# Kernel tuning notes

Hardware: AMD Instinct MI355X
Metric: run time of the kernel (lower is better)

Reference implementation:

```python
import jax, jax.numpy as jnp
import numpy as np

B, T, C = 4, 4096, 256

def setup_inputs() -> dict:
    key = jax.random.key(0)
    ks = jax.random.split(key, 7)
    s = 1.0 / np.sqrt(C)
    return {
        "x": jax.random.normal(ks[0], (B, T, C), dtype=jnp.float32),
        "Wq": jax.random.uniform(ks[1], (C, C), jnp.float32, -s, s),
        "bq": jax.random.uniform(ks[2], (C,), jnp.float32, -s, s),
        "Wk": jax.random.uniform(ks[3], (C, C), jnp.float32, -s, s),
        "bk": jax.random.uniform(ks[4], (C,), jnp.float32, -s, s),
        "Wv": jax.random.uniform(ks[5], (C, C), jnp.float32, -s, s),
        "bv": jax.random.uniform(ks[6], (C,), jnp.float32, -s, s),
    }

def reference(x, Wq, bq, Wk, bk, Wv, bv):
    # Projections (torch Linear: y = x @ W^T + b; here W stored as [in,out])
    q = x @ Wq + bq  # [B,T,C]
    k = x @ Wk + bk
    v = x @ Wv + bv
    dk = q.shape[-1]
    scores = jnp.einsum('btc,bsc->bts', q, k) / jnp.sqrt(jnp.float32(dk))
    Tn = x.shape[1]
    causal = jnp.tril(jnp.ones((Tn, Tn), dtype=bool))  # [T,T]
    scores = jnp.where(causal[None, :, :], scores, jnp.float32(-1e9))
    attn = jax.nn.softmax(scores, axis=-1)
    return jnp.einsum('bts,bsc->btc', attn, v)
```

## Files before the change

kernel.cpp:

```cpp
#include <hip/hip_runtime.h>
#include <hip/hip_bf16.h>

#define T_SEQ 4096
#define DIM   256
#define NBATCH 4

typedef short s8v __attribute__((ext_vector_type(8)));
typedef float f4v __attribute__((ext_vector_type(4)));
typedef unsigned short u16;

#define MFMA16(a,b,c) __builtin_amdgcn_mfma_f32_16x16x32_bf16(a,b,c,0,0,0)
#define FENCE_LGKM() asm volatile("s_waitcnt lgkmcnt(0)" ::: "memory")

__device__ int g_cnt[4];

static __device__ __forceinline__ u16 f2bf(float f) {
  union { float f; unsigned int u; } c; c.f = f;
  unsigned int u = c.u;
  unsigned int r = (u + 0x7fffu + ((u >> 16) & 1u)) >> 16;
  return (u16)r;
}

static __device__ __forceinline__ s8v pack8(const float* p) {
  float4 a = *(const float4*)p;
  float4 b = *(const float4*)(p + 4);
  s8v r;
  r[0] = (short)f2bf(a.x); r[1] = (short)f2bf(a.y);
  r[2] = (short)f2bf(a.z); r[3] = (short)f2bf(a.w);
  r[4] = (short)f2bf(b.x); r[5] = (short)f2bf(b.y);
  r[6] = (short)f2bf(b.z); r[7] = (short)f2bf(b.w);
  return r;
}

static __device__ __forceinline__ void gll16(const u16* g, u16* l) {
  __builtin_amdgcn_global_load_lds(
      (const __attribute__((address_space(1))) unsigned int*)g,
      (__attribute__((address_space(3))) unsigned int*)l, 16, 0, 0);
}

__global__ void diag_fill_kernel(float* __restrict__ out, float val, int n) {
  int i = blockIdx.x * blockDim.x + threadIdx.x;
  if (i < n) out[i] = val;
}

__global__ void wtrans_kernel(const float* __restrict__ Wq, const float* __restrict__ Wk,
                              const float* __restrict__ Wv, u16* __restrict__ Wt) {
  if (blockIdx.x == 0 && blockIdx.y == 0 && blockIdx.z == 0 &&
      threadIdx.y == 0 && threadIdx.x < 4)
    g_cnt[threadIdx.x] = 0;
  __shared__ float tile[32][33];
  int m = blockIdx.z;
  const float* W = (m == 0) ? Wq : ((m == 1) ? Wk : Wv);
  int bx = blockIdx.x * 32, by = blockIdx.y * 32;
  int x = threadIdx.x, y = threadIdx.y;
  #pragma unroll
  for (int i = 0; i < 32; i += 8) tile[y + i][x] = W[(by + y + i) * DIM + bx + x];
  __syncthreads();
  u16* o = Wt + m * DIM * DIM;
  #pragma unroll
  for (int i = 0; i < 32; i += 8) o[(bx + y + i) * DIM + by + x] = f2bf(tile[x][y + i]);
}

__global__ __launch_bounds__(256) void proj_kernel(
    const float* __restrict__ x, const u16* __restrict__ Wt,
    const float* __restrict__ bq, const float* __restrict__ bk, const float* __restrict__ bv,
    u16* __restrict__ qf, u16* __restrict__ kf, u16* __restrict__ vf) {
  alignas(16) __shared__ u16 Kl[64 * 264];
  alignas(16) __shared__ u16 Vl[256 * 72];

  int bid = blockIdx.x;
  int which = blockIdx.y;
  int tid  = threadIdx.x;
  int wave = tid >> 6, lane = tid & 63, quad = lane >> 4, l16 = lane & 15;
  int row0 = bid * 64 + wave * 16;

  s8v a[8];
  const float* xp = x + (size_t)(row0 + l16) * DIM + quad * 8;
  #pragma unroll
  for (int ks = 0; ks < 8; ks++) a[ks] = pack8(xp + ks * 32);

  if (which == 0) {
    const u16* W = Wt + DIM * DIM;
    f4v acc[16];
    #pragma unroll
    for (int nt = 0; nt < 16; nt++) acc[nt] = (f4v){0.f, 0.f, 0.f, 0.f};
    #pragma unroll
    for (int ks = 0; ks < 8; ks++) {
      #pragma unroll
      for (int nt = 0; nt < 16; nt++) {
        s8v bfr = *(const s8v*)(W + (nt * 16 + l16) * DIM + ks * 32 + quad * 8);
        acc[nt] = MFMA16(a[ks], bfr, acc[nt]);
      }
    }
    #pragma unroll
    for (int nt = 0; nt < 16; nt++) {
      float bb = bk[nt * 16 + l16];
      #pragma unroll
      for (int r = 0; r < 4; r++)
        Kl[(wave * 16 + quad * 4 + r) * 264 + nt * 16 + l16] = f2bf(acc[nt][r] + bb);
    }
    __syncthreads();
    #pragma unroll
    for (int i = 0; i < 8; i++) {
      int o = tid + i * 256;
      int tile = o >> 10, rem = o & 1023;
      int f = rem >> 6, ln = rem & 63;
      int sl = tile * 32 + (f >> 3) * 16 + (ln & 15);
      int c  = (f & 7) * 32 + (ln >> 4) * 8;
      s8v v = *(const s8v*)&Kl[sl * 264 + c];
      *(s8v*)&kf[(((size_t)(bid * 2 + tile) * 16 + f) * 64 + ln) * 8] = v;
    }
  } else if (which == 1) {
    const u16* W = Wt + 2 * DIM * DIM;
    f4v acc[16];
    #pragma unroll
    for (int nt = 0; nt < 16; nt++) acc[nt] = (f4v){0.f, 0.f, 0.f, 0.f};
    #pragma unroll
    for (int ks = 0; ks < 8; ks++) {
      #pragma unroll
      for (int nt = 0; nt < 16; nt++) {
        s8v bfr = *(const s8v*)(W + (nt * 16 + l16) * DIM + ks * 32 + quad * 8);
        acc[nt] = MFMA16(a[ks], bfr, acc[nt]);
      }
    }
    #pragma unroll
    for (int nt = 0; nt < 16; nt++) {
      float bb = bv[nt * 16 + l16];
      union { u16 h[4]; uint2 v2; } pk;
      #pragma unroll
      for (int r = 0; r < 4; r++) pk.h[r] = f2bf(acc[nt][r] + bb);
      *(uint2*)&Vl[(nt * 16 + l16) * 72 + wave * 16 + quad * 4] = pk.v2;
    }
    __syncthreads();
    #pragma unroll
    for (int i = 0; i < 8; i++) {
      int o = tid + i * 256;
      int tile = o >> 10, rem = o & 1023;
      int nt = rem >> 6, ln = rem & 63;
      int c  = nt * 16 + (ln & 15);
      int sl = tile * 32 + (ln >> 4) * 8;
      s8v v = *(const s8v*)&Vl[c * 72 + sl];
      *(s8v*)&vf[(((size_t)(bid * 2 + tile) * 16 + nt) * 64 + ln) * 8] = v;
    }
  } else {
    const u16* W = Wt;
    f4v acc[16];
    #pragma unroll
    for (int nt = 0; nt < 16; nt++) acc[nt] = (f4v){0.f, 0.f, 0.f, 0.f};
    #pragma unroll
    for (int ks = 0; ks < 8; ks++) {
      #pragma unroll
      for (int nt = 0; nt < 16; nt++) {
        s8v bfr = *(const s8v*)(W + (nt * 16 + l16) * DIM + ks * 32 + quad * 8);
        acc[nt] = MFMA16(a[ks], bfr, acc[nt]);
      }
    }
    #pragma unroll
    for (int nt = 0; nt < 16; nt++) {
      float bb = bq[nt * 16 + l16];
      #pragma unroll
      for (int r = 0; r < 4; r++)
        Kl[(wave * 16 + quad * 4 + r) * 264 + nt * 16 + l16] =
            f2bf((acc[nt][r] + bb) * 0.0625f);
    }
    __syncthreads();
    #pragma unroll
    for (int i = 0; i < 8; i++) {
      int o = tid + i * 256;
      int row = o >> 5, c8 = (o & 31) * 8;
      s8v v = *(const s8v*)&Kl[row * 264 + c8];
      int colp = (c8 + ((row & 31) << 3)) & 255;
      *(s8v*)&qf[(size_t)(bid * 64 + row) * 256 + colp] = v;
    }
  }
}

__global__ __launch_bounds__(1024, 4) void attn_kernel(
    const u16* __restrict__ qf, const u16* __restrict__ kf, const u16* __restrict__ vf,
    float* __restrict__ Opart, float* __restrict__ lpart, float* __restrict__ out) {
  alignas(16) __shared__ u16 Qs[32768];
  alignas(16) __shared__ u16 KVa[16384];
  alignas(16) __shared__ u16 KVb[16384];
  alignas(16) __shared__ u16 Ps[16 * 640];
  __shared__ int taskS;

  int bid = blockIdx.x, b = bid & 3;
  int tid = threadIdx.x;
  int w = tid >> 6, lane = tid & 63, quad = lane >> 4, l16 = lane & 15;
  int s = w >> 1, h = w & 1;

  const u16* qfb = qf + (size_t)b * T_SEQ * DIM;
  const u16* kfb = kf + (size_t)b * 128 * 8192;
  const u16* vfb = vf + (size_t)b * 128 * 8192;

  int qrow = (s << 4) + l16;
  int qbase = qrow << 8;
  int qrot = (qrow & 31) << 3;

  for (;;) {
    if (tid == 0) taskS = atomicAdd(&g_cnt[b], 1);
    __syncthreads();
    int t = taskS;
    if (t >= 80) break;
    int q, c;
    if (t < 8)        { q = 24 + t;        c = 0; }
    else if (t < 16)  { q = 24 + (t - 8);  c = 1; }
    else if (t < 24)  { q = 24 + (t - 16); c = 2; }
    else if (t == 24) { q = 31;            c = 3; }
    else if (t < 33)  { q = 16 + (t - 25); c = 0; }
    else if (t < 41)  { q = 16 + (t - 33); c = 1; }
    else if (t == 41) { q = 23;            c = 2; }
    else if (t < 50)  { q = 8 + (t - 42);  c = 0; }
    else if (t == 50) { q = 15;            c = 1; }
    else if (t == 51) { q = 7;             c = 0; }
    else { int u = t - 52, sz = u >> 2, band = u & 3;
           if (band == 0)      { q = 6 - sz;  c = 0; }
           else if (band == 1) { q = 14 - sz; c = 1; }
           else if (band == 2) { q = 22 - sz; c = 2; }
           else                { q = 30 - sz; c = 3; } }
    int row0 = q * 128;
    int n = 4 * q + 4;
    int lo = c * 32, hi = min(n, lo + 32);
    int nch = (q + 8) >> 3;

    {
      const u16* qsrc = qfb + ((size_t)row0 << 8) + (w << 11) + (lane << 3);
      u16* qdst = &Qs[w << 11];
      #pragma unroll
      for (int i = 0; i < 4; i++) gll16(qsrc + (i << 9), qdst + (i << 9));
      const u16* kt = kfb + ((size_t)lo << 13);
      const u16* vt = vfb + ((size_t)lo << 13);
      gll16(kt + (w << 9) + (lane << 3), &KVa[w << 9]);
      gll16(vt + (w << 9) + (lane << 3), &KVa[8192 + (w << 9)]);
    }
    __syncthreads();

    int rowBase = row0 + (s << 4);
    f4v o[8];
    #pragma unroll
    for (int nt = 0; nt < 8; nt++) o[nt] = (f4v){0.f, 0.f, 0.f, 0.f};
    float lrow[4] = {0.f, 0.f, 0.f, 0.f};

    auto iter_body = [&](const u16* buf, int kvi) {
      f4v c0 = (f4v){0.f, 0.f, 0.f, 0.f}, c1 = (f4v){0.f, 0.f, 0.f, 0.f};
      #pragma unroll
      for (int ks = 0; ks < 8; ks++) {
        s8v qa = *(const s8v*)&Qs[qbase + ((ks * 32 + (quad << 3) + qrot) & 255)];
        s8v k0 = *(const s8v*)&buf[(ks << 9) + (lane << 3)];
        s8v k1 = *(const s8v*)&buf[((8 + ks) << 9) + (lane << 3)];
        c0 = MFMA16(qa, k0, c0);
        c1 = MFMA16(qa, k1, c1);
      }
      int s0 = kvi * 32 + l16;
      #pragma unroll
      for (int r = 0; r < 4; r++) {
        int tq = rowBase + (quad << 2) + r;
        float v0 = (s0 > tq)      ? -1e30f : c0[r];
        float v1 = (s0 + 16 > tq) ? -1e30f : c1[r];
        float p0 = __expf(v0);
        float p1 = __expf(v1);
        Ps[w * 640 + ((quad << 2) + r) * 40 + l16]      = f2bf(p0);
        Ps[w * 640 + ((quad << 2) + r) * 40 + 16 + l16] = f2bf(p1);
        lrow[r] += p0 + p1;
      }
      FENCE_LGKM();
      s8v pa = *(const s8v*)&Ps[w * 640 + l16 * 40 + (quad << 3)];
      #pragma unroll
      for (int nt = 0; nt < 8; nt++) {
        s8v vfr = *(const s8v*)&buf[8192 + (((h << 3) + nt) << 9) + (lane << 3)];
        o[nt] = MFMA16(pa, vfr, o[nt]);
      }
    };

    #pragma unroll 1
    for (int kv = lo; kv < hi; kv += 2) {
      {
        const u16* kt = kfb + ((size_t)(kv + 1) << 13);
        const u16* vt = vfb + ((size_t)(kv + 1) << 13);
        gll16(kt + (w << 9) + (lane << 3), &KVb[w << 9]);
        gll16(vt + (w << 9) + (lane << 3), &KVb[8192 + (w << 9)]);
      }
      iter_body(KVa, kv);
      __syncthreads();
      if (kv + 2 < hi) {
        const u16* kt = kfb + ((size_t)(kv + 2) << 13);
        const u16* vt = vfb + ((size_t)(kv + 2) << 13);
        gll16(kt + (w << 9) + (lane << 3), &KVa[w << 9]);
        gll16(vt + (w << 9) + (lane << 3), &KVa[8192 + (w << 9)]);
      }
      iter_body(KVb, kv + 1);
      __syncthreads();
    }

    #pragma unroll
    for (int r = 0; r < 4; r++) {
      #pragma unroll
      for (int d = 1; d < 16; d <<= 1) lrow[r] += __shfl_xor(lrow[r], d);
    }

    if (nch == 1) {
      float inv[4];
      #pragma unroll
      for (int r = 0; r < 4; r++) inv[r] = 1.0f / lrow[r];
      #pragma unroll
      for (int nt = 0; nt < 8; nt++) {
        #pragma unroll
        for (int r = 0; r < 4; r++)
          out[(size_t)(b * T_SEQ + rowBase + (quad << 2) + r) * DIM +
              ((h * 8 + nt) * 16 + l16)] = o[nt][r] * inv[r];
      }
    } else {
      int slotB = (q < 16) ? (q - 8) * 2
                : (q < 24) ? 16 + (q - 16) * 3
                           : 40 + (q - 24) * 4;
      int slot = b * 72 + slotB + c;
      float* Op = Opart + ((size_t)slot << 15);
      #pragma unroll
      for (int nt = 0; nt < 8; nt++) {
        #pragma unroll
        for (int r = 0; r < 4; r++)
          Op[((s << 4) + (quad << 2) + r) * 256 + (h * 8 + nt) * 16 + l16] = o[nt][r];
      }
      if (h == 0 && l16 == 0) {
        #pragma unroll
        for (int r = 0; r < 4; r++)
          lpart[slot * 128 + (s << 4) + (quad << 2) + r] = lrow[r];
      }
    }
  }
}

__global__ void combine_kernel(const float* __restrict__ Opart,
                               const float* __restrict__ lpart,
                               float* __restrict__ out) {
  int blk = blockIdx.x;
  int b = blk & 3;
  int rest = blk >> 2;
  int q = 8 + (rest >> 3);
  int g = rest & 7;
  int col = threadIdx.x;
  int nch = (q + 8) >> 3;
  int slotB = (q < 16) ? (q - 8) * 2
            : (q < 24) ? 16 + (q - 16) * 3
                       : 40 + (q - 24) * 4;
  int slot0 = b * 72 + slotB;
  #pragma unroll 4
  for (int i = 0; i < 16; i++) {
    int rt = g * 16 + i;
    float acc = 0.f, ls = 0.f;
    for (int c = 0; c < nch; c++) {
      acc += Opart[(((size_t)(slot0 + c)) << 15) + rt * 256 + col];
      ls  += lpart[(slot0 + c) * 128 + rt];
    }
    out[(size_t)(b * T_SEQ + q * 128 + rt) * DIM + col] = acc / ls;
  }
}

extern "C" void kernel_launch(void* const* d_in, const int* in_sizes, int n_in,
                              void* d_out, int out_size, void* d_ws, size_t ws_size,
                              hipStream_t stream) {
  const float* x  = (const float*)d_in[0];
  const float* Wq = (const float*)d_in[1];
  const float* bq = (const float*)d_in[2];
  const float* Wk = (const float*)d_in[3];
  const float* bk = (const float*)d_in[4];
  const float* Wv = (const float*)d_in[5];
  const float* bv = (const float*)d_in[6];

  const size_t NTD = (size_t)NBATCH * T_SEQ * DIM;
  const size_t WT_ELEMS = (size_t)3 * DIM * DIM;
  const size_t NSLOT = 288;
  const size_t REQ_BYTES = (WT_ELEMS + 3 * NTD) * sizeof(u16)
                         + NSLOT * 32768 * sizeof(float)
                         + NSLOT * 128 * sizeof(float);

  if (ws_size < REQ_BYTES) {
    float val = (float)(ws_size >> 20);
    diag_fill_kernel<<<(out_size + 255) / 256, 256, 0, stream>>>((float*)d_out, val, out_size);
    return;
  }

  u16* ws = (u16*)d_ws;
  u16* WT = ws;
  u16* Kf = ws + WT_ELEMS;
  u16* Vf = Kf + NTD;
  u16* Qf = Vf + NTD;
  float* Opart = (float*)(Qf + NTD);
  float* lpart = Opart + NSLOT * 32768;

  wtrans_kernel<<<dim3(8, 8, 3), dim3(32, 8, 1), 0, stream>>>(Wq, Wk, Wv, WT);
  proj_kernel<<<dim3(256, 3, 1), dim3(256, 1, 1), 0, stream>>>(x, WT, bq, bk, bv, Qf, Kf, Vf);
  attn_kernel<<<dim3(256, 1, 1), dim3(1024, 1, 1), 0, stream>>>(Qf, Kf, Vf,
                                                                Opart, lpart, (float*)d_out);
  combine_kernel<<<dim3(768, 1, 1), dim3(256, 1, 1), 0, stream>>>(Opart, lpart, (float*)d_out);
}
```

Baseline: 227.9 us.

## Split QK^T across wave pairs and keep Q fragments in registers

The Q projection now writes Q in a pre-swizzled MFMA fragment layout, so each wave loads its eight Q fragments directly into registers and the Q shared-memory tile disappears. The two waves in a pair now each compute half of the 32 score columns instead of both computing all of them. This removes the duplicated QK^T MFMAs and the Q LDS reads, and frees shared memory. In exchange it adds a workgroup-wide s_barrier inside every KV iteration so the shared P tile is complete, and it merges row sums from the two halves through LDS.

```diff
diff --git a/kernel.cpp b/kernel.cpp
--- a/kernel.cpp
+++ b/kernel.cpp
@@ -167,10 +167,12 @@
     #pragma unroll
     for (int i = 0; i < 8; i++) {
       int o = tid + i * 256;
-      int row = o >> 5, c8 = (o & 31) * 8;
-      s8v v = *(const s8v*)&Kl[row * 264 + c8];
-      int colp = (c8 + ((row & 31) << 3)) & 255;
-      *(s8v*)&qf[(size_t)(bid * 64 + row) * 256 + colp] = v;
+      int tile = o >> 10, rem = o & 1023;
+      int f = rem >> 6, ln = rem & 63;
+      int sl = tile * 32 + (f >> 3) * 16 + (ln & 15);
+      int c  = (f & 7) * 32 + (ln >> 4) * 8;
+      s8v v = *(const s8v*)&Kl[sl * 264 + c];
+      *(s8v*)&qf[(((size_t)(bid * 2 + tile) * 16 + f) * 64 + ln) * 8] = v;
     }
   }
 }
@@ -178,10 +180,10 @@
 __global__ __launch_bounds__(1024, 4) void attn_kernel(
     const u16* __restrict__ qf, const u16* __restrict__ kf, const u16* __restrict__ vf,
     float* __restrict__ Opart, float* __restrict__ lpart, float* __restrict__ out) {
-  alignas(16) __shared__ u16 Qs[32768];
   alignas(16) __shared__ u16 KVa[16384];
   alignas(16) __shared__ u16 KVb[16384];
-  alignas(16) __shared__ u16 Ps[16 * 640];
+  alignas(16) __shared__ u16 Ps[8 * 640];
+  __shared__ float lbuf[8][2][16];
   __shared__ int taskS;
 
   int bid = blockIdx.x, b = bid & 3;
@@ -189,13 +191,9 @@
   int w = tid >> 6, lane = tid & 63, quad = lane >> 4, l16 = lane & 15;
   int s = w >> 1, h = w & 1;
 
-  const u16* qfb = qf + (size_t)b * T_SEQ * DIM;
+  const u16* qfb = qf + (size_t)b * 128 * 8192;
   const u16* kfb = kf + (size_t)b * 128 * 8192;
   const u16* vfb = vf + (size_t)b * 128 * 8192;
-
-  int qrow = (s << 4) + l16;
-  int qbase = qrow << 8;
-  int qrot = (qrow & 31) << 3;
 
   for (;;) {
     if (tid == 0) taskS = atomicAdd(&g_cnt[b], 1);
@@ -223,11 +221,14 @@
     int lo = c * 32, hi = min(n, lo + 32);
     int nch = (q + 8) >> 3;
 
+    s8v qa[8];
     {
-      const u16* qsrc = qfb + ((size_t)row0 << 8) + (w << 11) + (lane << 3);
-      u16* qdst = &Qs[w << 11];
-      #pragma unroll
-      for (int i = 0; i < 4; i++) gll16(qsrc + (i << 9), qdst + (i << 9));
+      const u16* qt = qfb + (((size_t)(q * 4 + (s >> 1)) * 16 + (s & 1) * 8) * 64) * 8;
+      #pragma unroll
+      for (int ks = 0; ks < 8; ks++) qa[ks] = *(const s8v*)(qt + (ks * 64 + lane) * 8);
+    }
+
+    {
       const u16* kt = kfb + ((size_t)lo << 13);
       const u16* vt = vfb + ((size_t)lo << 13);
       gll16(kt + (w << 9) + (lane << 3), &KVa[w << 9]);
@@ -242,29 +243,25 @@
     float lrow[4] = {0.f, 0.f, 0.f, 0.f};
 
     auto iter_body = [&](const u16* buf, int kvi) {
-      f4v c0 = (f4v){0.f, 0.f, 0.f, 0.f}, c1 = (f4v){0.f, 0.f, 0.f, 0.f};
+      f4v cc = (f4v){0.f, 0.f, 0.f, 0.f};
       #pragma unroll
       for (int ks = 0; ks < 8; ks++) {
-        s8v qa = *(const s8v*)&Qs[qbase + ((ks * 32 + (quad << 3) + qrot) & 255)];
-        s8v k0 = *(const s8v*)&buf[(ks << 9) + (lane << 3)];
-        s8v k1 = *(const s8v*)&buf[((8 + ks) << 9) + (lane << 3)];
-        c0 = MFMA16(qa, k0, c0);
-        c1 = MFMA16(qa, k1, c1);
-      }
-      int s0 = kvi * 32 + l16;
+        s8v kfr = *(const s8v*)&buf[(((h << 3) + ks) << 9) + (lane << 3)];
+        cc = MFMA16(qa[ks], kfr, cc);
+      }
+      int s0 = kvi * 32 + (h << 4) + l16;
       #pragma unroll
       for (int r = 0; r < 4; r++) {
         int tq = rowBase + (quad << 2) + r;
-        float v0 = (s0 > tq)      ? -1e30f : c0[r];
-        float v1 = (s0 + 16 > tq) ? -1e30f : c1[r];
-        float p0 = __expf(v0);
-        float p1 = __expf(v1);
-        Ps[w * 640 + ((quad << 2) + r) * 40 + l16]      = f2bf(p0);
-        Ps[w * 640 + ((quad << 2) + r) * 40 + 16 + l16] = f2bf(p1);
-        lrow[r] += p0 + p1;
+        float p = __expf((s0 > tq) ? -1e30f : cc[r]);
+        Ps[s * 640 + ((quad << 2) + r) * 40 + (h << 4) + l16] = f2bf(p);
+        lrow[r] += p;
       }
       FENCE_LGKM();
-      s8v pa = *(const s8v*)&Ps[w * 640 + l16 * 40 + (quad << 3)];
+      __builtin_amdgcn_sched_barrier(0);
+      __builtin_amdgcn_s_barrier();
+      __builtin_amdgcn_sched_barrier(0);
+      s8v pa = *(const s8v*)&Ps[s * 640 + l16 * 40 + (quad << 3)];
       #pragma unroll
       for (int nt = 0; nt < 8; nt++) {
         s8v vfr = *(const s8v*)&buf[8192 + (((h << 3) + nt) << 9) + (lane << 3)];
@@ -297,17 +294,21 @@
       #pragma unroll
       for (int d = 1; d < 16; d <<= 1) lrow[r] += __shfl_xor(lrow[r], d);
     }
+    if (l16 == 0) {
+      #pragma unroll
+      for (int r = 0; r < 4; r++) lbuf[s][h][(quad << 2) + r] = lrow[r];
+    }
+    __syncthreads();
 
     if (nch == 1) {
-      float inv[4];
-      #pragma unroll
-      for (int r = 0; r < 4; r++) inv[r] = 1.0f / lrow[r];
       #pragma unroll
       for (int nt = 0; nt < 8; nt++) {
         #pragma unroll
-        for (int r = 0; r < 4; r++)
+        for (int r = 0; r < 4; r++) {
+          float ls = lbuf[s][0][(quad << 2) + r] + lbuf[s][1][(quad << 2) + r];
           out[(size_t)(b * T_SEQ + rowBase + (quad << 2) + r) * DIM +
-              ((h * 8 + nt) * 16 + l16)] = o[nt][r] * inv[r];
+              ((h * 8 + nt) * 16 + l16)] = o[nt][r] / ls;
+        }
       }
     } else {
       int slotB = (q < 16) ? (q - 8) * 2
@@ -324,7 +325,8 @@
       if (h == 0 && l16 == 0) {
         #pragma unroll
         for (int r = 0; r < 4; r++)
-          lpart[slot * 128 + (s << 4) + (quad << 2) + r] = lrow[r];
+          lpart[slot * 128 + (s << 4) + (quad << 2) + r] =
+              lbuf[s][0][(quad << 2) + r] + lbuf[s][1][(quad << 2) + r];
       }
     }
   }
```

Result: faster. 212.2 us (-6.9%).
